# Optimization experiments

Measured on AMD Instinct MI355X. Metric: run time of the kernel, lower is better.

Reference implementation:

```python
import jax, jax.numpy as jnp
import numpy as np


def setup_inputs() -> dict:
    key = jax.random.key(0)
    ks = jax.random.split(key, 12)
    B, D, H, T, K = 12288, 1024, 512, 12, 3
    s = 0.02  # weight init scale for numerical stability
    return {
        "x": jax.random.normal(ks[0], (B, D), jnp.float32),
        "Wp": jax.random.normal(ks[1], (H, D), jnp.float32) * s,
        "bp": jnp.zeros((H,), jnp.float32),
        "opW1": jax.random.normal(ks[2], (T, K, H, H), jnp.float32) * s,
        "opb1": jnp.zeros((T, K, H), jnp.float32),
        "opW2": jax.random.normal(ks[3], (T, K, H, H), jnp.float32) * s,
        "opb2": jnp.zeros((T, K, H), jnp.float32),
        "op_logits": jax.random.normal(ks[4], (T, K), jnp.float32) * 0.1,
        "id_emb": jax.random.normal(ks[5], (T, 4), jnp.float32),
        "rW1": jax.random.normal(ks[6], (H, H + 7), jnp.float32) * s,
        "rb1": jnp.zeros((H,), jnp.float32),
        "rW2": jax.random.normal(ks[7], (T + 1, H), jnp.float32) * s,
        "rb2": jnp.zeros((T + 1,), jnp.float32),
        "gW1": jax.random.normal(ks[8], (T, H, 7), jnp.float32) * s,
        "gb1": jnp.zeros((T, H), jnp.float32),
        "gW2": jax.random.normal(ks[9], (T, 2, H), jnp.float32) * s,
        "gb2": jnp.zeros((T, 2), jnp.float32),
        "phW": jax.random.normal(ks[10], (D, H), jnp.float32) * s,
        "phb": jnp.zeros((D,), jnp.float32),
        "noise": jax.random.normal(ks[11], (B, H), jnp.float32),
    }


def reference(x, Wp, bp, opW1, opb1, opW2, opb2, op_logits, id_emb,
              rW1, rb1, rW2, rb2, gW1, gb1, gW2, gb2, phW, phb, noise):
    T, K, H, _ = opW1.shape
    B = x.shape[0]
    g = B // T  # balanced deterministic routing: patch p -> temper p % T

    # input projection (patch_size == hidden_dim => patches == x_proj)
    xp = x @ Wp.T + bp                                   # [B, H]
    xg = xp.reshape(g, T, H).transpose(1, 0, 2)           # [T, g, H]

    # Temper.apply_operators: softmax-weighted sum of Linear-ReLU-Linear-ReLU ops
    w = jax.nn.softmax(op_logits, axis=-1)                # [T, K]
    h1 = jax.nn.relu(jnp.einsum('tgj,tkij->tkgi', xg, opW1) + opb1[:, :, None, :])
    h2 = jax.nn.relu(jnp.einsum('tkgj,tkij->tkgi', h1, opW2) + opb2[:, :, None, :])
    out = jnp.einsum('tk,tkgi->tgi', w, h2)               # [T, g, H]
    # freshness buffers start at 0 -> fresh-bonus branch inactive

    usage = w                                             # usage starts at 0, += w
    conflict = jnp.std(w, axis=-1, ddof=1)                # torch.std is unbiased
    plast_t = ((out - xg) ** 2).mean(axis=(1, 2))         # last_plasticity per temper

    # IntrinsicGrowthController.compute_intrinsic_signals (buffers at init values)
    ng = noise.reshape(g, T, H).transpose(1, 0, 2) * 0.01
    plasticity = (ng ** 2).mean(-1)                       # [T, g] ((out_noisy-out)^2)
    novelty = (xg ** 2).mean(-1)                          # input_mean == 0
    pred_err = ((out - xg) ** 2).mean(-1)
    up = usage / (usage.sum(-1, keepdims=True) + 1e-6)
    entropy = -(up * jnp.log(jnp.clip(up, 1e-6, None))).sum(-1)   # [T]
    sparsity = jnp.abs(out).mean(-1)
    reward_delta = -pred_err                              # moving avg starts at 0
    new_avg = 0.01 * pred_err.mean(-1)                    # updated moving avg
    reward_var = ((pred_err - new_avg[:, None]) ** 2).mean(-1)
    signals = jnp.stack([plasticity.mean(-1), novelty.mean(-1), pred_err.mean(-1),
                         entropy, sparsity.mean(-1), reward_delta.mean(-1),
                         reward_var], axis=-1)            # [T, 7]

    # growth controller MLP 7 -> H -> 2 (per temper)
    gc_h = jax.nn.relu(jnp.einsum('thj,tj->th', gW1, signals) + gb1)
    decision = jnp.einsum('toh,th->to', gW2, gc_h) + gb2  # [T, 2] (grow, prune)

    # enriched routing input: [out | id_embed(4) | novelty | conflict | plasticity]
    nov_e = jnp.broadcast_to(signals[:, 1][:, None, None], (T, g, 1))
    conf_e = jnp.broadcast_to(conflict[:, None, None], (T, g, 1))
    plas_e = jnp.broadcast_to(plast_t[:, None, None], (T, g, 1))
    ide = jnp.broadcast_to(id_emb[:, None, :], (T, g, id_emb.shape[1]))
    enriched = jnp.concatenate([out, ide, nov_e, conf_e, plas_e], axis=-1)  # [T,g,H+7]

    rh = jax.nn.relu(jnp.einsum('tgj,ij->tgi', enriched, rW1) + rb1)
    logits = jnp.einsum('tgj,ij->tgi', rh, rW2) + rb2     # [T, g, T+1]

    # scatter back to original patch order (inverse of the grouping reshape)
    out_full = out.transpose(1, 0, 2).reshape(B, H)
    logits_full = logits.transpose(1, 0, 2).reshape(B, T + 1)
    pred = out_full @ phW.T + phb                         # predictive head [B, D]
    return (out_full, logits_full, pred, decision)
```

## Files before the change

### kernel.cpp

```cpp
#include <hip/hip_runtime.h>

typedef unsigned short u16;
typedef float f32x4 __attribute__((ext_vector_type(4)));
typedef float f32x8 __attribute__((ext_vector_type(8)));
typedef u16   u16x4 __attribute__((ext_vector_type(4)));
typedef u16   u16x8 __attribute__((ext_vector_type(8)));
typedef __bf16 bf16x8 __attribute__((ext_vector_type(8)));

#define WS_W       0u
#define WS_BIASRH  512u
#define WS_WPB     25600u
#define WS_PHWB    1074176u
#define WS_RW1B    2122752u
#define WS_W1B     2647040u
#define WS_W2B     21521408u
#define WS_XPB     40395776u
#define WS_H1B     52978688u
#define WS_OUTB    90727424u
#define WS_RHB     103310336u

#define OUT_LG   6291456
#define OUT_PRED 6451200
#define OUT_DEC  19034112

__device__ __forceinline__ u16 f2bf(float f) {
    unsigned u = __builtin_bit_cast(unsigned, f);
    return (u16)((u + 0x7FFFu + ((u >> 16) & 1u)) >> 16);
}
__device__ __forceinline__ float bf2f(u16 h) {
    return __builtin_bit_cast(float, (unsigned)h << 16);
}

typedef __attribute__((address_space(1))) void* gas1p;
typedef __attribute__((address_space(3))) void* las3p;
__device__ __forceinline__ void gload16(const u16* g, u16* l) {
    __builtin_amdgcn_global_load_lds((gas1p)(unsigned long long)g,
                                     (las3p)(unsigned)(unsigned long long)l,
                                     16, 0, 0);
}

__device__ __forceinline__ void zero_acc(f32x4 (&a)[4][4]) {
#pragma unroll
    for (int i = 0; i < 4; i++)
#pragma unroll
        for (int j = 0; j < 4; j++)
            a[i][j] = (f32x4){0.f, 0.f, 0.f, 0.f};
}

__device__ __forceinline__ void mfma_loop(
    const u16* __restrict__ Ab, size_t pa,
    const u16* __restrict__ Bb, size_t pb,
    int K, u16* sA, u16* sB, f32x4 (&acc)[4][4])
{
    const int tid = threadIdx.x;
    const int l = tid & 63, wv = tid >> 6;
    const int wm = (wv >> 1) * 64, wn = (wv & 1) * 64;
    const int m16 = l & 15, k8 = l >> 4;
    const int kc = (tid & 3) * 8;
    const size_t ra0 = (size_t)(tid >> 2) * pa + kc;
    const size_t ra1 = ra0 + 64 * pa;
    const size_t rb0 = (size_t)(tid >> 2) * pb + kc;
    const size_t rb1 = rb0 + 64 * pb;
    const int aO = (wm + m16) * 32 + k8 * 8;
    const int bO = (wn + m16) * 32 + k8 * 8;
    gload16(Ab + ra0, sA + tid * 8);
    gload16(Ab + ra1, sA + (tid + 256) * 8);
    gload16(Bb + rb0, sB + tid * 8);
    gload16(Bb + rb1, sB + (tid + 256) * 8);
    int cur = 0;
    for (int kt = 0; kt < K; kt += 32) {
        __builtin_amdgcn_s_barrier();
        const int nx = cur ^ 1;
        if (kt + 32 < K) {
            const int kn = kt + 32;
            gload16(Ab + ra0 + kn, sA + nx * 4096 + tid * 8);
            gload16(Ab + ra1 + kn, sA + nx * 4096 + (tid + 256) * 8);
            gload16(Bb + rb0 + kn, sB + nx * 4096 + tid * 8);
            gload16(Bb + rb1 + kn, sB + nx * 4096 + (tid + 256) * 8);
            asm volatile("s_waitcnt vmcnt(4)" ::: "memory");
        } else {
            asm volatile("s_waitcnt vmcnt(0)" ::: "memory");
        }
        __builtin_amdgcn_s_barrier();
        const u16* cA = sA + cur * 4096;
        const u16* cB = sB + cur * 4096;
        bf16x8 af[4], bv[4];
#pragma unroll
        for (int i = 0; i < 4; i++) af[i] = *(const bf16x8*)(cA + aO + i * 512);
#pragma unroll
        for (int i = 0; i < 4; i++) bv[i] = *(const bf16x8*)(cB + bO + i * 512);
#pragma unroll
        for (int i = 0; i < 4; i++)
#pragma unroll
            for (int j = 0; j < 4; j++)
                acc[i][j] = __builtin_amdgcn_mfma_f32_16x16x32_bf16(af[i], bv[j], acc[i][j], 0, 0, 0);
        cur = nx;
    }
}

__device__ __forceinline__ void mfma_loop64(
    const u16* __restrict__ Ab, size_t pa,
    const u16* __restrict__ Bb, size_t pb,
    int K, u16* sA, u16* sB, f32x4 (&acc)[4][2])
{
    const int tid = threadIdx.x;
    const int l = tid & 63, wv = tid >> 6;
    const int m16 = l & 15, k8 = l >> 4;
    const int kc = (tid & 3) * 8;
    const size_t ra0 = (size_t)(tid >> 2) * pa + kc;
    const size_t rb0 = (size_t)(tid >> 2) * pb + kc;
    const size_t rb1 = rb0 + 64 * pb;
    const int aO = m16 * 32 + k8 * 8;
    const int bO = (wv * 32 + m16) * 32 + k8 * 8;
    gload16(Ab + ra0, sA + tid * 8);
    gload16(Bb + rb0, sB + tid * 8);
    gload16(Bb + rb1, sB + (tid + 256) * 8);
    int cur = 0;
    for (int kt = 0; kt < K; kt += 32) {
        __builtin_amdgcn_s_barrier();
        const int nx = cur ^ 1;
        if (kt + 32 < K) {
            const int kn = kt + 32;
            gload16(Ab + ra0 + kn, sA + nx * 2048 + tid * 8);
            gload16(Bb + rb0 + kn, sB + nx * 4096 + tid * 8);
            gload16(Bb + rb1 + kn, sB + nx * 4096 + (tid + 256) * 8);
            asm volatile("s_waitcnt vmcnt(3)" ::: "memory");
        } else {
            asm volatile("s_waitcnt vmcnt(0)" ::: "memory");
        }
        __builtin_amdgcn_s_barrier();
        const u16* cA = sA + cur * 2048;
        const u16* cB = sB + cur * 4096;
        bf16x8 af[4], bv[2];
#pragma unroll
        for (int i = 0; i < 4; i++) af[i] = *(const bf16x8*)(cA + aO + i * 512);
#pragma unroll
        for (int j = 0; j < 2; j++) bv[j] = *(const bf16x8*)(cB + bO + j * 512);
#pragma unroll
        for (int i = 0; i < 4; i++)
#pragma unroll
            for (int j = 0; j < 2; j++)
                acc[i][j] = __builtin_amdgcn_mfma_f32_16x16x32_bf16(af[i], bv[j], acc[i][j], 0, 0, 0);
        cur = nx;
    }
}

__global__ __launch_bounds__(256) void cvt6(
    const float* __restrict__ opW1, u16* __restrict__ w1b,
    const float* __restrict__ opW2, u16* __restrict__ w2b,
    const float* __restrict__ Wp,   u16* __restrict__ wpb,
    const float* __restrict__ phW,  u16* __restrict__ phwb,
    const float* __restrict__ rW1,  u16* __restrict__ rw1b,
    const float* __restrict__ op_logits, float* __restrict__ wbuf)
{
    if (blockIdx.x == 0 && threadIdx.x < 12) {
        const int t = threadIdx.x;
        float l0 = op_logits[t*3+0], l1 = op_logits[t*3+1], l2 = op_logits[t*3+2];
        float mx = fmaxf(l0, fmaxf(l1, l2));
        float e0 = expf(l0-mx), e1 = expf(l1-mx), e2 = expf(l2-mx);
        float inv = 1.f / (e0 + e1 + e2);
        wbuf[t*3+0] = e0*inv; wbuf[t*3+1] = e1*inv; wbuf[t*3+2] = e2*inv;
    }
    int i = (blockIdx.x * 256 + threadIdx.x) * 4;
    const float* s; u16* d;
    if (i < 9437184)                    { s = opW1; d = w1b; }
    else if ((i -= 9437184) < 9437184)  { s = opW2; d = w2b; }
    else if ((i -= 9437184) < 524288)   { s = Wp;   d = wpb; }
    else if ((i -= 524288)  < 524288)   { s = phW;  d = phwb; }
    else {
        i -= 524288;
        int row = i >> 9, j = i & 511;
        const float* sr = rW1 + (size_t)row * 519 + j;
        u16x4 o = { f2bf(sr[0]), f2bf(sr[1]), f2bf(sr[2]), f2bf(sr[3]) };
        *(u16x4*)(rw1b + i) = o;
        return;
    }
    f32x4 v = *(const f32x4*)(s + i);
    u16x4 o = { f2bf(v[0]), f2bf(v[1]), f2bf(v[2]), f2bf(v[3]) };
    *(u16x4*)(d + i) = o;
}

__global__ __launch_bounds__(256) void kgemm_xp(
    const float* __restrict__ x, const u16* __restrict__ wpb,
    const float* __restrict__ bp, u16* __restrict__ xpb)
{
    __shared__ u16 sA[4096], sB[8192];
    const int rowBase = blockIdx.y * 64, colBase = blockIdx.x * 128;
    const int tid = threadIdx.x, l = tid & 63, wv = tid >> 6;
    const int m16 = l & 15, k8 = l >> 4;
    const int kc = (tid & 3) * 8;
    const float* xrow = x + (size_t)(rowBase + (tid >> 2)) * 1024 + kc;
    const u16* Bb = wpb + (size_t)colBase * 1024;
    const size_t rb0 = (size_t)(tid >> 2) * 1024 + kc;
    const size_t rb1 = rb0 + 64 * 1024;
    const int aO = m16 * 32 + k8 * 8;
    const int bO = (wv * 32 + m16) * 32 + k8 * 8;
    f32x4 acc[4][2];
#pragma unroll
    for (int i = 0; i < 4; i++)
#pragma unroll
        for (int j = 0; j < 2; j++) acc[i][j] = (f32x4){0.f,0.f,0.f,0.f};

    gload16(Bb + rb0, sB + tid * 8);
    gload16(Bb + rb1, sB + (tid + 256) * 8);
    {
        f32x8 a0 = *(const f32x8*)(xrow);
        u16x8 c;
#pragma unroll
        for (int j = 0; j < 8; j++) c[j] = f2bf(a0[j]);
        *(u16x8*)(sA + tid * 8) = c;
    }
    f32x8 avR = *(const f32x8*)(xrow + 32);
    asm volatile("s_waitcnt lgkmcnt(0)" ::: "memory");

    int cur = 0;
    for (int kt = 0; kt < 1024; kt += 32) {
        __builtin_amdgcn_s_barrier();
        const int nx = cur ^ 1;
        if (kt + 32 < 1024) {
            gload16(Bb + rb0 + kt + 32, sB + nx * 4096 + tid * 8);
            gload16(Bb + rb1 + kt + 32, sB + nx * 4096 + (tid + 256) * 8);
            u16x8 c;
#pragma unroll
            for (int j = 0; j < 8; j++) c[j] = f2bf(avR[j]);
            *(u16x8*)(sA + nx * 2048 + tid * 8) = c;
            avR = *(const f32x8*)(xrow + ((kt + 64) & 1023));
            asm volatile("s_waitcnt lgkmcnt(0)" ::: "memory");
        } else {
            asm volatile("s_waitcnt vmcnt(0) lgkmcnt(0)" ::: "memory");
        }
        __builtin_amdgcn_s_barrier();
        const u16* cA = sA + cur * 2048;
        const u16* cB = sB + cur * 4096;
        bf16x8 af[4], bv[2];
#pragma unroll
        for (int i = 0; i < 4; i++) af[i] = *(const bf16x8*)(cA + aO + i * 512);
#pragma unroll
        for (int j = 0; j < 2; j++) bv[j] = *(const bf16x8*)(cB + bO + j * 512);
#pragma unroll
        for (int i = 0; i < 4; i++)
#pragma unroll
            for (int j = 0; j < 2; j++)
                acc[i][j] = __builtin_amdgcn_mfma_f32_16x16x32_bf16(af[i], bv[j], acc[i][j], 0, 0, 0);
        cur = nx;
    }
#pragma unroll
    for (int in = 0; in < 2; in++) {
        const int gc = colBase + wv * 32 + in * 16 + m16;
        const float bv = bp[gc];
#pragma unroll
        for (int im = 0; im < 4; im++) {
            const int gr = rowBase + im * 16 + k8 * 4;
#pragma unroll
            for (int r = 0; r < 4; r++)
                xpb[(size_t)(gr + r) * 512 + gc] = f2bf(acc[im][in][r] + bv);
        }
    }
}

__global__ __launch_bounds__(256) void kgemm_h1(
    const u16* __restrict__ xpb, const u16* __restrict__ w1b,
    const float* __restrict__ opb1, u16* __restrict__ h1b)
{
    __shared__ u16 sA[8192], sB[8192];
    const int seg = blockIdx.z, t = seg / 3;
    const int rowBase = blockIdx.y * 128, colBase = blockIdx.x * 128;
    f32x4 acc[4][4]; zero_acc(acc);
    mfma_loop(xpb + (size_t)rowBase * 6144 + (size_t)t * 512, 6144,
              w1b + (size_t)seg * 262144 + (size_t)colBase * 512, 512, 512, sA, sB, acc);
    const int tid = threadIdx.x, l = tid & 63, wv = tid >> 6;
    const int wm = (wv >> 1) * 64, wn = (wv & 1) * 64, m16 = l & 15, k8 = l >> 4;
    u16* hseg = h1b + (size_t)seg * 524288;
#pragma unroll
    for (int in = 0; in < 4; in++) {
        const int gc = colBase + wn + in * 16 + m16;
        const float bv = opb1[seg * 512 + gc];
#pragma unroll
        for (int im = 0; im < 4; im++) {
            const int gr = rowBase + wm + im * 16 + k8 * 4;
#pragma unroll
            for (int r = 0; r < 4; r++)
                hseg[(size_t)(gr + r) * 512 + gc] = f2bf(fmaxf(acc[im][in][r] + bv, 0.f));
        }
    }
}

__global__ __launch_bounds__(256) void kgemm_out(
    const u16* __restrict__ h1b, const u16* __restrict__ w2b,
    const float* __restrict__ opb2, const float* __restrict__ wbuf,
    float* __restrict__ outF, u16* __restrict__ outb)
{
    __shared__ u16 sA[4096], sB[8192];
    const int t = blockIdx.z;
    const int rowBase = blockIdx.y * 64, colBase = blockIdx.x * 128;
    const int tid = threadIdx.x, l = tid & 63, wv = tid >> 6;
    const int m16 = l & 15, k8 = l >> 4;
    float oac[4][2][4];
#pragma unroll
    for (int i = 0; i < 4; i++)
#pragma unroll
        for (int j = 0; j < 2; j++)
#pragma unroll
            for (int r = 0; r < 4; r++) oac[i][j][r] = 0.f;

    for (int kk = 0; kk < 3; kk++) {
        const int seg = t * 3 + kk;
        f32x4 acc[4][2];
#pragma unroll
        for (int i = 0; i < 4; i++)
#pragma unroll
            for (int j = 0; j < 2; j++) acc[i][j] = (f32x4){0.f,0.f,0.f,0.f};
        mfma_loop64(h1b + ((size_t)seg * 1024 + rowBase) * 512, 512,
                    w2b + (size_t)seg * 262144 + (size_t)colBase * 512, 512, 512, sA, sB, acc);
        const float wk = wbuf[seg];
#pragma unroll
        for (int in = 0; in < 2; in++) {
            const float bv = opb2[seg * 512 + colBase + wv * 32 + in * 16 + m16];
#pragma unroll
            for (int im = 0; im < 4; im++)
#pragma unroll
                for (int r = 0; r < 4; r++)
                    oac[im][in][r] += wk * fmaxf(acc[im][in][r] + bv, 0.f);
        }
    }
#pragma unroll
    for (int im = 0; im < 4; im++)
#pragma unroll
        for (int r = 0; r < 4; r++) {
            const int gi = rowBase + im * 16 + k8 * 4 + r;
            const size_t b = (size_t)gi * 12 + t;
#pragma unroll
            for (int in = 0; in < 2; in++) {
                const int gc = colBase + wv * 32 + in * 16 + m16;
                const float v = oac[im][in][r];
                outF[b * 512 + gc] = v;
                outb[b * 512 + gc] = f2bf(v);
            }
        }
}

__global__ __launch_bounds__(256) void kgemm_predrh(
    const u16* __restrict__ outb, const u16* __restrict__ phwb,
    const float* __restrict__ phb, const u16* __restrict__ rw1b,
    const float* __restrict__ bias_rh, float* __restrict__ outPred,
    u16* __restrict__ rhb)
{
    __shared__ u16 sA[8192], sB[8192];
    const int bz = blockIdx.x;
    const int rowBase = blockIdx.y * 128;
    const bool isPred = bz < 8;
    const int colBase = (isPred ? bz : bz - 8) * 128;
    const u16* Bb = isPred ? (phwb + (size_t)colBase * 512)
                           : (rw1b + (size_t)colBase * 512);
    f32x4 acc[4][4]; zero_acc(acc);
    mfma_loop(outb + (size_t)rowBase * 512, 512, Bb, 512, 512, sA, sB, acc);
    const int tid = threadIdx.x, l = tid & 63, wv = tid >> 6;
    const int wm = (wv >> 1) * 64, wn = (wv & 1) * 64, m16 = l & 15, k8 = l >> 4;
    if (isPred) {
#pragma unroll
        for (int in = 0; in < 4; in++) {
            const int gc = colBase + wn + in * 16 + m16;
            const float bv = phb[gc];
#pragma unroll
            for (int im = 0; im < 4; im++) {
                const int gr = rowBase + wm + im * 16 + k8 * 4;
#pragma unroll
                for (int r = 0; r < 4; r++)
                    outPred[(size_t)(gr + r) * 1024 + gc] = acc[im][in][r] + bv;
            }
        }
    } else {
#pragma unroll
        for (int in = 0; in < 4; in++) {
            const int gc = colBase + wn + in * 16 + m16;
#pragma unroll
            for (int im = 0; im < 4; im++) {
                const int gr = rowBase + wm + im * 16 + k8 * 4;
#pragma unroll
                for (int r = 0; r < 4; r++) {
                    const int b = gr + r;
                    const float bv = bias_rh[(b % 12) * 512 + gc];
                    rhb[(size_t)b * 512 + gc] = f2bf(fmaxf(acc[im][in][r] + bv, 0.f));
                }
            }
        }
    }
}

__global__ __launch_bounds__(256) void rowred(
    const float* __restrict__ outF, const u16* __restrict__ xpb,
    const float* __restrict__ noise, float* __restrict__ partials)
{
    const int tid = threadIdx.x, l = tid & 63, wv = tid >> 6;
    const int gw = blockIdx.x * 4 + wv;
    const size_t base = (size_t)gw * 12 * 512 + l * 8;
    float* pout = partials + (size_t)gw * 60;
#pragma unroll
    for (int t = 0; t < 12; t++) {
        const size_t off = base + (size_t)t * 512;
        f32x8 ov = *(const f32x8*)(outF + off);
        f32x8 nv = *(const f32x8*)(noise + off);
        u16x8 xv = *(const u16x8*)(xpb + off);
        float s1 = 0, s2 = 0, s3 = 0, s4 = 0;
#pragma unroll
        for (int j = 0; j < 8; j++) {
            float xg = bf2f(xv[j]);
            float o = ov[j];
            float d = o - xg;
            s1 += d * d; s2 += xg * xg; s3 += fabsf(o); s4 += nv[j] * nv[j];
        }
#pragma unroll
        for (int off2 = 32; off2 > 0; off2 >>= 1) {
            s1 += __shfl_xor(s1, off2);
            s2 += __shfl_xor(s2, off2);
            s3 += __shfl_xor(s3, off2);
            s4 += __shfl_xor(s4, off2);
        }
        if (l < 5) {
            float v = (l == 0) ? s1 : (l == 1) ? s2 : (l == 2) ? s3
                    : (l == 3) ? s4 : s1 * s1;
            pout[t * 5 + l] = v;
        }
    }
}

__global__ __launch_bounds__(256) void sig_kernel(
    const float* __restrict__ op_logits, const float* __restrict__ id_emb,
    const float* __restrict__ rW1, const float* __restrict__ rb1,
    const float* __restrict__ gW1, const float* __restrict__ gb1,
    const float* __restrict__ gW2, const float* __restrict__ gb2,
    const float* __restrict__ partials, float* __restrict__ bias_rh,
    float* __restrict__ outDec)
{
    const int t = blockIdx.x, tid = threadIdx.x;
    __shared__ float sig[7], ex7[7], gch[512], red[256], accv[5];
    float a[5] = {0.f, 0.f, 0.f, 0.f, 0.f};
    for (int g = tid; g < 1024; g += 256) {
        const float* p = partials + (size_t)g * 60 + t * 5;
#pragma unroll
        for (int s = 0; s < 5; s++) a[s] += p[s];
    }
#pragma unroll
    for (int s = 0; s < 5; s++) {
        red[tid] = a[s]; __syncthreads();
        for (int k = 128; k > 0; k >>= 1) { if (tid < k) red[tid] += red[tid + k]; __syncthreads(); }
        if (tid == 0) accv[s] = red[0];
        __syncthreads();
    }
    if (tid == 0) {
        float l0 = op_logits[t*3+0], l1 = op_logits[t*3+1], l2 = op_logits[t*3+2];
        float mx = fmaxf(l0, fmaxf(l1, l2));
        float e0 = expf(l0-mx), e1 = expf(l1-mx), e2 = expf(l2-mx);
        float es = e0 + e1 + e2;
        float w0 = e0/es, w1 = e1/es, w2 = e2/es;
        float mean = (w0 + w1 + w2) * (1.f/3.f);
        float var = ((w0-mean)*(w0-mean) + (w1-mean)*(w1-mean) + (w2-mean)*(w2-mean)) * 0.5f;
        float conflict = sqrtf(var);
        float inv_s = 1.f / (w0 + w1 + w2 + 1e-6f);
        float u0 = w0*inv_s, u1 = w1*inv_s, u2 = w2*inv_s;
        float ent = -(u0*logf(fmaxf(u0,1e-6f)) + u1*logf(fmaxf(u1,1e-6f)) + u2*logf(fmaxf(u2,1e-6f)));
        const float inv = 1.f / (1024.f * 512.f);
        float plast = accv[0] * inv;
        float nov   = accv[1] * inv;
        float spars = accv[2] * inv;
        float plasticity = 1e-4f * accv[3] * inv;
        float pe2 = accv[4] * (1.f / (1024.f * 512.f * 512.f));
        float na = 0.01f * plast;
        float rvar = pe2 - 2.f*na*plast + na*na;
        sig[0]=plasticity; sig[1]=nov; sig[2]=plast; sig[3]=ent; sig[4]=spars; sig[5]=-plast; sig[6]=rvar;
        ex7[0]=id_emb[t*4+0]; ex7[1]=id_emb[t*4+1]; ex7[2]=id_emb[t*4+2]; ex7[3]=id_emb[t*4+3];
        ex7[4]=nov; ex7[5]=conflict; ex7[6]=plast;
    }
    __syncthreads();
    for (int h = tid; h < 512; h += 256) {
        float aa = gb1[t*512 + h];
#pragma unroll
        for (int j = 0; j < 7; j++) aa += gW1[(t*512 + h)*7 + j] * sig[j];
        gch[h] = fmaxf(aa, 0.f);
        float bb = rb1[h];
#pragma unroll
        for (int e = 0; e < 7; e++) bb += ex7[e] * rW1[(size_t)h * 519 + 512 + e];
        bias_rh[t*512 + h] = bb;
    }
    __syncthreads();
    float p0 = 0.f, p1 = 0.f;
    for (int h = tid; h < 512; h += 256) {
        p0 += gW2[(t*2 + 0)*512 + h] * gch[h];
        p1 += gW2[(t*2 + 1)*512 + h] * gch[h];
    }
    red[tid] = p0; __syncthreads();
    for (int s = 128; s > 0; s >>= 1) { if (tid < s) red[tid] += red[tid + s]; __syncthreads(); }
    if (tid == 0) outDec[t*2 + 0] = red[0] + gb2[t*2 + 0];
    __syncthreads();
    red[tid] = p1; __syncthreads();
    for (int s = 128; s > 0; s >>= 1) { if (tid < s) red[tid] += red[tid + s]; __syncthreads(); }
    if (tid == 0) outDec[t*2 + 1] = red[0] + gb2[t*2 + 1];
}

__global__ __launch_bounds__(256) void logits_kernel(
    const u16* __restrict__ rhb, const float* __restrict__ rW2,
    const float* __restrict__ rb2, float* __restrict__ outLg)
{
    __shared__ float T2[512 * 13];
    __shared__ float rb2s[16];
    const int tid = threadIdx.x;
    for (int i = tid; i < 6656; i += 256) {
        int o = i >> 9, j = i & 511;
        T2[j * 13 + o] = rW2[i];
    }
    if (tid < 13) rb2s[tid] = rb2[tid];
    __syncthreads();
    const int l = tid & 63, wv = tid >> 6;
    const size_t b = (size_t)blockIdx.x * 4 + wv;
    const u16* rrow = rhb + b * 512;
    float rv[8];
#pragma unroll
    for (int jj = 0; jj < 8; jj++) rv[jj] = bf2f(rrow[l + 64 * jj]);
    float p[13];
#pragma unroll
    for (int o = 0; o < 13; o++) p[o] = 0.f;
#pragma unroll
    for (int jj = 0; jj < 8; jj++) {
        const float* tp = T2 + (l + 64 * jj) * 13;
#pragma unroll
        for (int o = 0; o < 13; o++) p[o] += rv[jj] * tp[o];
    }
#pragma unroll
    for (int o = 0; o < 13; o++) {
#pragma unroll
        for (int off = 32; off > 0; off >>= 1) p[o] += __shfl_xor(p[o], off);
    }
    if (l == 0) {
        float* orow = outLg + b * 13;
#pragma unroll
        for (int o = 0; o < 13; o++) orow[o] = p[o] + rb2s[o];
    }
}

extern "C" void kernel_launch(void* const* d_in, const int* in_sizes, int n_in,
                              void* d_out, int out_size, void* d_ws, size_t ws_size,
                              hipStream_t stream)
{
    const float* x         = (const float*)d_in[0];
    const float* Wp        = (const float*)d_in[1];
    const float* bp        = (const float*)d_in[2];
    const float* opW1      = (const float*)d_in[3];
    const float* opb1      = (const float*)d_in[4];
    const float* opW2      = (const float*)d_in[5];
    const float* opb2      = (const float*)d_in[6];
    const float* op_logits = (const float*)d_in[7];
    const float* id_emb    = (const float*)d_in[8];
    const float* rW1       = (const float*)d_in[9];
    const float* rb1       = (const float*)d_in[10];
    const float* rW2       = (const float*)d_in[11];
    const float* rb2       = (const float*)d_in[12];
    const float* gW1       = (const float*)d_in[13];
    const float* gb1       = (const float*)d_in[14];
    const float* gW2       = (const float*)d_in[15];
    const float* gb2       = (const float*)d_in[16];
    const float* phW       = (const float*)d_in[17];
    const float* phb       = (const float*)d_in[18];
    const float* noise     = (const float*)d_in[19];

    char* ws = (char*)d_ws;
    float* wbuf    = (float*)(ws + WS_W);
    float* bias_rh = (float*)(ws + WS_BIASRH);
    u16* wpb  = (u16*)(ws + WS_WPB);
    u16* phwb = (u16*)(ws + WS_PHWB);
    u16* rw1b = (u16*)(ws + WS_RW1B);
    u16* w1b  = (u16*)(ws + WS_W1B);
    u16* w2b  = (u16*)(ws + WS_W2B);
    u16* xpb  = (u16*)(ws + WS_XPB);
    u16* h1b  = (u16*)(ws + WS_H1B);
    u16* outb = (u16*)(ws + WS_OUTB);
    u16* rhb  = (u16*)(ws + WS_RHB);
    float* partials = (float*)(ws + WS_W1B);

    float* outF    = (float*)d_out;
    float* outLg   = outF + OUT_LG;
    float* outPred = outF + OUT_PRED;
    float* outDec  = outF + OUT_DEC;

    cvt6<<<19712, 256, 0, stream>>>(opW1, w1b, opW2, w2b, Wp, wpb,
                                    phW, phwb, rW1, rw1b, op_logits, wbuf);
    kgemm_xp  <<<dim3(4, 192),    256, 0, stream>>>(x, wpb, bp, xpb);
    kgemm_h1  <<<dim3(4, 8, 36),  256, 0, stream>>>(xpb, w1b, opb1, h1b);
    kgemm_out <<<dim3(4, 16, 12), 256, 0, stream>>>(h1b, w2b, opb2, wbuf, outF, outb);
    rowred    <<<256,             256, 0, stream>>>(outF, xpb, noise, partials);
    sig_kernel<<<12,              256, 0, stream>>>(op_logits, id_emb, rW1, rb1, gW1, gb1,
                                                    gW2, gb2, partials, bias_rh, outDec);
    kgemm_predrh<<<dim3(12, 96),  256, 0, stream>>>(outb, phwb, phb, rw1b, bias_rh,
                                                    outPred, rhb);
    logits_kernel<<<3072,         256, 0, stream>>>(rhb, rW2, rb2, outLg);
}
```

Measured before the change: 398.0 us.

## Swizzle GEMM block order for cache locality and deepen xp prefetch pipeline

Switches the four GEMM kernels from multi-dimensional grids to 1D grids with a remapped block-to-tile order. Nearby block IDs now share A rows and B columns, which is meant to improve L2 reuse across blocks running at the same time. kgemm_xp also unrolls its K loop by two with alternating fp32 x-row registers, prefetching two steps ahead and using a partial vmcnt wait instead of draining loads. The extra prefetch register raises register pressure, and the vmcnt(4) count has to match the number of outstanding loads for correctness.

Measured after the change: 394.5 us. About the same (-0.9%).

```diff
diff --git a/kernel.cpp b/kernel.cpp
--- a/kernel.cpp
+++ b/kernel.cpp
@@ -180,12 +180,38 @@
     *(u16x4*)(d + i) = o;
 }
 
+#define XP_STEP(KT, REG, CUR) do {                                              \
+    __builtin_amdgcn_s_barrier();                                               \
+    gload16(Bb + rb0 + (KT) + 32, sB + (1-(CUR)) * 4096 + tid * 8);             \
+    gload16(Bb + rb1 + (KT) + 32, sB + (1-(CUR)) * 4096 + (tid + 256) * 8);     \
+    { u16x8 c_;                                                                 \
+      _Pragma("unroll") for (int j_ = 0; j_ < 8; j_++) c_[j_] = f2bf(REG[j_]);  \
+      *(u16x8*)(sA + (1-(CUR)) * 2048 + tid * 8) = c_; }                        \
+    REG = *(const f32x8*)(xrow + (((KT) + 96) & 1023));                         \
+    asm volatile("s_waitcnt lgkmcnt(0)" ::: "memory");                          \
+    asm volatile("s_waitcnt vmcnt(4)" ::: "memory");                            \
+    __builtin_amdgcn_s_barrier();                                               \
+    { const u16* cA_ = sA + (CUR) * 2048; const u16* cB_ = sB + (CUR) * 4096;   \
+      bf16x8 af_[4], bv_[2];                                                    \
+      _Pragma("unroll") for (int i_ = 0; i_ < 4; i_++)                          \
+          af_[i_] = *(const bf16x8*)(cA_ + aO + i_ * 512);                      \
+      _Pragma("unroll") for (int j_ = 0; j_ < 2; j_++)                          \
+          bv_[j_] = *(const bf16x8*)(cB_ + bO + j_ * 512);                      \
+      _Pragma("unroll") for (int i_ = 0; i_ < 4; i_++)                          \
+      _Pragma("unroll") for (int j_ = 0; j_ < 2; j_++)                          \
+          acc[i_][j_] = __builtin_amdgcn_mfma_f32_16x16x32_bf16(                \
+              af_[i_], bv_[j_], acc[i_][j_], 0, 0, 0); }                        \
+} while (0)
+
 __global__ __launch_bounds__(256) void kgemm_xp(
     const float* __restrict__ x, const u16* __restrict__ wpb,
     const float* __restrict__ bp, u16* __restrict__ xpb)
 {
     __shared__ u16 sA[4096], sB[8192];
-    const int rowBase = blockIdx.y * 64, colBase = blockIdx.x * 128;
+    const int id = blockIdx.x;
+    const int cb = (id >> 3) & 3;
+    const int yb = (id & 7) + ((id >> 5) << 3);
+    const int rowBase = yb * 64, colBase = cb * 128;
     const int tid = threadIdx.x, l = tid & 63, wv = tid >> 6;
     const int m16 = l & 15, k8 = l >> 4;
     const int kc = (tid & 3) * 8;
@@ -210,28 +236,21 @@
         for (int j = 0; j < 8; j++) c[j] = f2bf(a0[j]);
         *(u16x8*)(sA + tid * 8) = c;
     }
-    f32x8 avR = *(const f32x8*)(xrow + 32);
+    f32x8 rEv = *(const f32x8*)(xrow + 32);
+    f32x8 rOd = *(const f32x8*)(xrow + 64);
     asm volatile("s_waitcnt lgkmcnt(0)" ::: "memory");
 
-    int cur = 0;
-    for (int kt = 0; kt < 1024; kt += 32) {
-        __builtin_amdgcn_s_barrier();
-        const int nx = cur ^ 1;
-        if (kt + 32 < 1024) {
-            gload16(Bb + rb0 + kt + 32, sB + nx * 4096 + tid * 8);
-            gload16(Bb + rb1 + kt + 32, sB + nx * 4096 + (tid + 256) * 8);
-            u16x8 c;
-#pragma unroll
-            for (int j = 0; j < 8; j++) c[j] = f2bf(avR[j]);
-            *(u16x8*)(sA + nx * 2048 + tid * 8) = c;
-            avR = *(const f32x8*)(xrow + ((kt + 64) & 1023));
-            asm volatile("s_waitcnt lgkmcnt(0)" ::: "memory");
-        } else {
-            asm volatile("s_waitcnt vmcnt(0) lgkmcnt(0)" ::: "memory");
-        }
-        __builtin_amdgcn_s_barrier();
-        const u16* cA = sA + cur * 2048;
-        const u16* cB = sB + cur * 4096;
+    for (int kt = 0; kt < 960; kt += 64) {
+        XP_STEP(kt, rEv, 0);
+        XP_STEP(kt + 32, rOd, 1);
+    }
+    XP_STEP(960, rEv, 0);
+    __builtin_amdgcn_s_barrier();
+    asm volatile("s_waitcnt vmcnt(0) lgkmcnt(0)" ::: "memory");
+    __builtin_amdgcn_s_barrier();
+    {
+        const u16* cA = sA + 2048;
+        const u16* cB = sB + 4096;
         bf16x8 af[4], bv[2];
 #pragma unroll
         for (int i = 0; i < 4; i++) af[i] = *(const bf16x8*)(cA + aO + i * 512);
@@ -242,7 +261,6 @@
 #pragma unroll
             for (int j = 0; j < 2; j++)
                 acc[i][j] = __builtin_amdgcn_mfma_f32_16x16x32_bf16(af[i], bv[j], acc[i][j], 0, 0, 0);
-        cur = nx;
     }
 #pragma unroll
     for (int in = 0; in < 2; in++) {
@@ -263,8 +281,11 @@
     const float* __restrict__ opb1, u16* __restrict__ h1b)
 {
     __shared__ u16 sA[8192], sB[8192];
-    const int seg = blockIdx.z, t = seg / 3;
-    const int rowBase = blockIdx.y * 128, colBase = blockIdx.x * 128;
+    const int id = blockIdx.x;
+    const int seg = id >> 5, i = id & 31, t = seg / 3;
+    const int xb = i & 3;
+    const int yb = (i >> 3) + ((i >> 2) & 1) * 4;
+    const int rowBase = yb * 128, colBase = xb * 128;
     f32x4 acc[4][4]; zero_acc(acc);
     mfma_loop(xpb + (size_t)rowBase * 6144 + (size_t)t * 512, 6144,
               w1b + (size_t)seg * 262144 + (size_t)colBase * 512, 512, 512, sA, sB, acc);
@@ -291,25 +312,28 @@
     float* __restrict__ outF, u16* __restrict__ outb)
 {
     __shared__ u16 sA[4096], sB[8192];
-    const int t = blockIdx.z;
-    const int rowBase = blockIdx.y * 64, colBase = blockIdx.x * 128;
+    const int id = blockIdx.x;
+    const int t = id >> 6, i = id & 63;
+    const int a = i & 1, b2i = (i >> 1) & 3, q = i >> 3;
+    const int xb = 2 * a + (q & 1), yb = 4 * b2i + (q >> 1);
+    const int rowBase = yb * 64, colBase = xb * 128;
     const int tid = threadIdx.x, l = tid & 63, wv = tid >> 6;
     const int m16 = l & 15, k8 = l >> 4;
     float oac[4][2][4];
 #pragma unroll
-    for (int i = 0; i < 4; i++)
+    for (int i1 = 0; i1 < 4; i1++)
 #pragma unroll
         for (int j = 0; j < 2; j++)
 #pragma unroll
-            for (int r = 0; r < 4; r++) oac[i][j][r] = 0.f;
+            for (int r = 0; r < 4; r++) oac[i1][j][r] = 0.f;
 
     for (int kk = 0; kk < 3; kk++) {
         const int seg = t * 3 + kk;
         f32x4 acc[4][2];
 #pragma unroll
-        for (int i = 0; i < 4; i++)
-#pragma unroll
-            for (int j = 0; j < 2; j++) acc[i][j] = (f32x4){0.f,0.f,0.f,0.f};
+        for (int i1 = 0; i1 < 4; i1++)
+#pragma unroll
+            for (int j = 0; j < 2; j++) acc[i1][j] = (f32x4){0.f,0.f,0.f,0.f};
         mfma_loop64(h1b + ((size_t)seg * 1024 + rowBase) * 512, 512,
                     w2b + (size_t)seg * 262144 + (size_t)colBase * 512, 512, 512, sA, sB, acc);
         const float wk = wbuf[seg];
@@ -346,8 +370,11 @@
     u16* __restrict__ rhb)
 {
     __shared__ u16 sA[8192], sB[8192];
-    const int bz = blockIdx.x;
-    const int rowBase = blockIdx.y * 128;
+    const int id = blockIdx.x;
+    const int j = id >> 3;
+    const int bz = j % 12;
+    const int yb = (id & 7) + (j / 12) * 8;
+    const int rowBase = yb * 128;
     const bool isPred = bz < 8;
     const int colBase = (isPred ? bz : bz - 8) * 128;
     const u16* Bb = isPred ? (phwb + (size_t)colBase * 512)
@@ -583,13 +610,13 @@
 
     cvt6<<<19712, 256, 0, stream>>>(opW1, w1b, opW2, w2b, Wp, wpb,
                                     phW, phwb, rW1, rw1b, op_logits, wbuf);
-    kgemm_xp  <<<dim3(4, 192),    256, 0, stream>>>(x, wpb, bp, xpb);
-    kgemm_h1  <<<dim3(4, 8, 36),  256, 0, stream>>>(xpb, w1b, opb1, h1b);
-    kgemm_out <<<dim3(4, 16, 12), 256, 0, stream>>>(h1b, w2b, opb2, wbuf, outF, outb);
-    rowred    <<<256,             256, 0, stream>>>(outF, xpb, noise, partials);
-    sig_kernel<<<12,              256, 0, stream>>>(op_logits, id_emb, rW1, rb1, gW1, gb1,
-                                                    gW2, gb2, partials, bias_rh, outDec);
-    kgemm_predrh<<<dim3(12, 96),  256, 0, stream>>>(outb, phwb, phb, rw1b, bias_rh,
-                                                    outPred, rhb);
-    logits_kernel<<<3072,         256, 0, stream>>>(rhb, rW2, rb2, outLg);
-}
+    kgemm_xp  <<<768,  256, 0, stream>>>(x, wpb, bp, xpb);
+    kgemm_h1  <<<1152, 256, 0, stream>>>(xpb, w1b, opb1, h1b);
+    kgemm_out <<<768,  256, 0, stream>>>(h1b, w2b, opb2, wbuf, outF, outb);
+    rowred    <<<256,  256, 0, stream>>>(outF, xpb, noise, partials);
+    sig_kernel<<<12,   256, 0, stream>>>(op_logits, id_emb, rW1, rb1, gW1, gb1,
+                                         gW2, gb2, partials, bias_rh, outDec);
+    kgemm_predrh<<<1152, 256, 0, stream>>>(outb, phwb, phb, rw1b, bias_rh,
+                                           outPred, rhb);
+    logits_kernel<<<3072, 256, 0, stream>>>(rhb, rW2, rb2, outLg);
+}
```
